# Kernel optimization log

Hardware: AMD Instinct MI355X
Metric: run time of the kernel (lower is better)

## Reference

```python
import jax, jax.numpy as jnp
import numpy as np

N = 4096
F = 256
E = 65536
NEG = -1e30  # mask value for non-neighbors in distance top-k


def setup_inputs() -> dict:
    key = jax.random.key(0)
    k1, k2, k3, k4, k5 = jax.random.split(key, 5)
    edge_index = jax.random.randint(k1, (2, E), 0, N)
    edge_weight = jax.random.uniform(k2, (E,), dtype=jnp.float32)
    features = jax.random.normal(k3, (N, F), dtype=jnp.float32)
    theta_1 = jax.random.uniform(k4, (1,), dtype=jnp.float32)
    theta_2 = jax.random.uniform(k5, (1,), dtype=jnp.float32)
    return {"edge_index": edge_index, "edge_weight": edge_weight,
            "features": features, "theta_1": theta_1, "theta_2": theta_2}


def reference(edge_index, edge_weight, features, theta_1, theta_2):
    n = features.shape[0]
    row, col = edge_index[0], edge_index[1]
    # Adjacency construction is done on detached numpy in the original.
    w = jax.lax.stop_gradient(edge_weight)
    X = jax.lax.stop_gradient(features)
    # sp.csr_matrix sums duplicate (i,j) entries -> scatter-add; + I; clamp >1 to 1
    A = jnp.zeros((n, n), jnp.float32).at[row, col].add(w)
    A = A + jnp.eye(n, dtype=jnp.float32)
    A = jnp.where(A > 1.0, 1.0, A)
    A2 = A @ A  # adjs[1] = sp_A ** 2
    # generate_sparse_ids mutates both A and A_robust(=A2 for r=2) with setdiag(0)
    off = 1.0 - jnp.eye(n, dtype=jnp.float32)
    A = A * off
    A2 = A2 * off
    D = jnp.sum(A != 0.0, axis=1)    # per-node degree (count_nonzero)
    Dr = jnp.sum(A2 != 0.0, axis=1)  # robust (2-hop) degree
    Df = D.astype(jnp.float32)
    d_thres = jnp.mean(Df) + 2.0 * jnp.std(Df)  # euclidean metric branch
    # squared-euclidean distances via gram trick: ||xu - xv||^2
    sq = jnp.sum(X * X, axis=1)
    dist2 = sq[:, None] + sq[None, :] - 2.0 * (X @ X.T)
    nbr2 = A2 != 0.0  # A_robust neighbors (diag excluded, already zeroed)
    dmask = jnp.where(nbr2, dist2, NEG)
    # rank of each candidate in descending-distance order (stable argsort)
    order = jnp.argsort(-dmask, axis=1)
    rank = jnp.argsort(order, axis=1)
    # nz_sel = D_r[u] - round(sparse_rate * D[u]) with sparse_rate=2.0 (exact ints)
    nz_sel = Dr - 2 * D
    # faithful to numpy argsort()[-0:] which selects ALL neighbors when nz_sel==0
    nz_eff = jnp.where(nz_sel == 0, n, nz_sel)
    Z_sparse = nbr2 & (rank < nz_eff[:, None])  # top nz_sel farthest neighbors
    Z_high = A == 0.0  # highD branch: zero all non-1-hop-neighbors
    highD = Df > d_thres
    nosparse = (~highD) & (2 * D > Dr)  # empty sparse_ids branch
    Z = jnp.where(highD[:, None], Z_high,
                  jnp.where(nosparse[:, None], False, Z_sparse))
    adj_k = jnp.where(Z, 0.0, A2 - A)  # diag already zero in both
    vals = theta_1 * edge_weight + theta_2 * jax.lax.stop_gradient(adj_k[row, col])
    return jnp.clip(vals, 0.0, None)
```

## Files before the change

### kernel.cpp

```cpp
#include <hip/hip_runtime.h>

#define NN 4096
#define FF 256
#define EE 65536
#define MAXDEG 64
#define MAXEPR 256
#define NCAND 2048

__device__ __forceinline__ int wred_sum(int v) {
#pragma unroll
    for (int o = 32; o >= 1; o >>= 1) v += __shfl_xor(v, o);
    return v;
}

__global__ void k_scatter(const int* __restrict__ ei, int* __restrict__ ecnt,
                          int* __restrict__ elist) {
    int e = blockIdx.x * blockDim.x + threadIdx.x;
    if (e >= EE) return;
    int r = ei[e];
    int p = atomicAdd(&ecnt[r], 1);
    if (p < MAXEPR) elist[r * MAXEPR + p] = e;
}

__global__ void k_build(const int* __restrict__ ei, const float* __restrict__ ew,
                        const int* __restrict__ ecnt, const int* __restrict__ elist,
                        const float* __restrict__ X,
                        unsigned short* __restrict__ ccol, float* __restrict__ cval,
                        int* __restrict__ deg, double* __restrict__ sq) {
    __shared__ float row[NN];
    __shared__ int cnt;
    const int u = blockIdx.x;
    const int tid = threadIdx.x;
    const int lane = tid & 63;
    const unsigned long long lmask = (1ull << lane) - 1ull;

    for (int i = tid; i < NN; i += 256) row[i] = 0.f;
    if (tid == 0) cnt = 0;
    __syncthreads();

    int ne = ecnt[u]; if (ne > MAXEPR) ne = MAXEPR;
    for (int i = tid; i < ne; i += 256) {
        int e = elist[u * MAXEPR + i];
        int c = ei[EE + e];
        if (c != u) atomicAdd(&row[c], ew[e]);
    }
    __syncthreads();

    for (int i = tid; i < NN; i += 256) {
        float w = row[i];
        bool nzf = (w != 0.f);
        unsigned long long m = __ballot(nzf);
        int base = 0;
        if (lane == 0 && m) base = atomicAdd(&cnt, __popcll(m));
        base = __shfl(base, 0);
        int pos = base + __popcll(m & lmask);
        if (nzf && pos < MAXDEG) {
            ccol[u * MAXDEG + pos] = (unsigned short)i;
            cval[u * MAXDEG + pos] = fminf(w, 1.f);
        }
    }
    __syncthreads();
    if (tid == 0) deg[u] = cnt;

    if (tid < 64) {
        float4 x4 = ((const float4*)(X + (size_t)u * FF))[lane];
        double s = (double)x4.x * x4.x + (double)x4.y * x4.y +
                   (double)x4.z * x4.z + (double)x4.w * x4.w;
#pragma unroll
        for (int o = 32; o >= 1; o >>= 1) s += __shfl_xor(s, o);
        if (lane == 0) sq[u] = s;
    }
}

__global__ void k_stats(const int* __restrict__ deg, double* __restrict__ thres) {
    __shared__ double sd[256], sd2[256];
    int t = threadIdx.x;
    double s = 0, s2 = 0;
    for (int i = t; i < NN; i += 256) {
        double d = (double)deg[i];
        s += d; s2 += d * d;
    }
    sd[t] = s; sd2[t] = s2;
    __syncthreads();
    for (int o = 128; o >= 1; o >>= 1) {
        if (t < o) { sd[t] += sd[t + o]; sd2[t] += sd2[t + o]; }
        __syncthreads();
    }
    if (t == 0) {
        double mean = sd[0] / NN;
        double var = sd2[0] / NN - mean * mean;
        if (var < 0) var = 0;
        thres[0] = mean + 2.0 * sqrt(var);
    }
}

__launch_bounds__(256, 5)
__global__ void k_main(const int* __restrict__ ei, const float* __restrict__ ew,
                       const float* __restrict__ X, const float* __restrict__ th1p,
                       const float* __restrict__ th2p,
                       const unsigned short* __restrict__ ccol,
                       const float* __restrict__ cval, const int* __restrict__ deg,
                       const int* __restrict__ ecnt, const int* __restrict__ elist,
                       const double* __restrict__ sq, const double* __restrict__ thresp,
                       float* __restrict__ out) {
    __shared__ float acc[NN];
    __shared__ float Xu[FF];
    __shared__ unsigned short cidx[NCAND];
    __shared__ float cdist[NCAND];
    __shared__ unsigned short Aucol[MAXDEG];
    __shared__ float Auval[MAXDEG];
    __shared__ int ncand;

    const int u = blockIdx.x;
    const int tid = threadIdx.x;
    const int lane = tid & 63;
    const int wave = tid >> 6;
    const unsigned long long lmask = (1ull << lane) - 1ull;

    const int du = deg[u];
    const int dul = min(du, MAXDEG);
    for (int i = tid; i < NN; i += 256) acc[i] = 0.f;
    if (tid < FF / 4)
        ((float4*)Xu)[tid] = ((const float4*)(X + (size_t)u * FF))[tid];
    if (tid >= 128 && tid - 128 < dul) {
        Aucol[tid - 128] = ccol[u * MAXDEG + tid - 128];
        Auval[tid - 128] = cval[u * MAXDEG + tid - 128];
    }
    if (tid == 0) ncand = 0;
    __syncthreads();

    for (int kk = wave; kk <= dul; kk += 4) {
        int k; float wuk;
        if (kk == dul) { k = u; wuk = 1.f; }
        else { k = Aucol[kk]; wuk = Auval[kk]; }
        int dkl = min(deg[k], MAXDEG);
        for (int j = lane; j <= dkl; j += 64) {
            int v; float wkv;
            if (j == dkl) { v = k; wkv = 1.f; }
            else { v = ccol[k * MAXDEG + j]; wkv = cval[k * MAXDEG + j]; }
            atomicAdd(&acc[v], wuk * wkv);
        }
    }
    __syncthreads();
    if (tid == 0) acc[u] = 0.f;
    __syncthreads();

    for (int i = tid; i < NN; i += 256) {
        bool nzf = (acc[i] != 0.f);
        unsigned long long m = __ballot(nzf);
        int base = 0;
        if (lane == 0 && m) base = atomicAdd(&ncand, __popcll(m));
        base = __shfl(base, 0);
        int pos = base + __popcll(m & lmask);
        if (nzf && pos < NCAND) cidx[pos] = (unsigned short)i;
    }
    __syncthreads();
    const int Dr = ncand;
    const int Drs = min(Dr, NCAND);

    const double squ = sq[u];
    for (int c = tid; c < Drs; c += 256) {
        int v = cidx[c];
        const float4* __restrict__ Xv = (const float4*)(X + (size_t)v * FF);
        double sqv = sq[v];
        double s0 = 0, s1 = 0, s2 = 0, s3 = 0;
#pragma unroll 2
        for (int f = 0; f < FF / 4; f += 4) {
            float4 a0 = Xv[f + 0], a1 = Xv[f + 1], a2 = Xv[f + 2], a3 = Xv[f + 3];
            float4 b0 = ((const float4*)Xu)[f + 0];
            float4 b1 = ((const float4*)Xu)[f + 1];
            float4 b2 = ((const float4*)Xu)[f + 2];
            float4 b3 = ((const float4*)Xu)[f + 3];
            s0 += (double)a0.x * b0.x + (double)a0.y * b0.y +
                  (double)a0.z * b0.z + (double)a0.w * b0.w;
            s1 += (double)a1.x * b1.x + (double)a1.y * b1.y +
                  (double)a1.z * b1.z + (double)a1.w * b1.w;
            s2 += (double)a2.x * b2.x + (double)a2.y * b2.y +
                  (double)a2.z * b2.z + (double)a2.w * b2.w;
            s3 += (double)a3.x * b3.x + (double)a3.y * b3.y +
                  (double)a3.z * b3.z + (double)a3.w * b3.w;
        }
        cdist[c] = (float)(squ + sqv - 2.0 * (s0 + s1 + s2 + s3));
    }
    __syncthreads();

    const int D = du;
    const bool highD = ((double)D > thresp[0]);
    const int nz = Dr - 2 * D;
    const float th1 = th1p[0], th2 = th2p[0];
    int ne = ecnt[u]; if (ne > MAXEPR) ne = MAXEPR;
    for (int idx = wave; idx < ne; idx += 4) {
        int e = elist[u * MAXEPR + idx];
        int v = ei[EE + e];
        float w = ew[e];
        float a2v = acc[v];
        float avl = 0.f;
        bool hit = false;
        for (int t = lane; t < dul; t += 64)
            if ((int)Aucol[t] == v) { avl = Auval[t]; hit = true; }
        unsigned long long hm = __ballot(hit);
        float av = hm ? __shfl(avl, (int)__builtin_ctzll(hm)) : 0.f;
        float adj;
        if (highD) {
            adj = (av != 0.f) ? (a2v - av) : 0.f;
        } else if (nz < 0) {
            adj = a2v - av;
        } else if (nz == 0) {
            adj = 0.f;
        } else if (a2v == 0.f) {
            adj = 0.f;
        } else {
            float dvl = 0.f; bool fnd = false;
            for (int c = lane; c < Drs; c += 64)
                if ((int)cidx[c] == v) { dvl = cdist[c]; fnd = true; }
            unsigned long long fm = __ballot(fnd);
            float dv = __shfl(dvl, (int)__builtin_ctzll(fm));
            int cnt = 0;
            for (int c = lane; c < Drs; c += 64) {
                float cd = cdist[c];
                int ci = cidx[c];
                cnt += (cd > dv || (cd == dv && ci < v)) ? 1 : 0;
            }
            cnt = wred_sum(cnt);
            adj = (cnt < nz) ? 0.f : (a2v - av);
        }
        if (lane == 0) out[e] = fmaxf(0.f, fmaf(th1, w, th2 * adj));
    }
}

extern "C" void kernel_launch(void* const* d_in, const int* in_sizes, int n_in,
                              void* d_out, int out_size, void* d_ws, size_t ws_size,
                              hipStream_t stream) {
    const int* ei = (const int*)d_in[0];
    const float* ew = (const float*)d_in[1];
    const float* X = (const float*)d_in[2];
    const float* th1 = (const float*)d_in[3];
    const float* th2 = (const float*)d_in[4];
    float* out = (float*)d_out;

    char* ws = (char*)d_ws;
    size_t off = 0;
    unsigned short* ccol = (unsigned short*)(ws + off); off += (size_t)NN * MAXDEG * 2;
    float* cval = (float*)(ws + off);         off += (size_t)NN * MAXDEG * 4;
    int* deg = (int*)(ws + off);              off += (size_t)NN * 4;
    int* ecnt = (int*)(ws + off);             off += (size_t)NN * 4;
    double* sq = (double*)(ws + off);         off += (size_t)NN * 8;
    double* thres = (double*)(ws + off);      off += 256;
    int* elist = (int*)(ws + off);            off += (size_t)NN * MAXEPR * 4;

    hipMemsetAsync(ecnt, 0, (size_t)NN * 4, stream);

    k_scatter<<<EE / 256, 256, 0, stream>>>(ei, ecnt, elist);
    k_build<<<NN, 256, 0, stream>>>(ei, ew, ecnt, elist, X, ccol, cval, deg, sq);
    k_stats<<<1, 256, 0, stream>>>(deg, thres);
    k_main<<<NN, 256, 0, stream>>>(ei, ew, X, th1, th2, ccol, cval, deg,
                                   ecnt, elist, sq, thres, out);
}
```

Before: 277.5 us.

## Split main kernel into A² pass and distance-rank pass, sparsify row build

The single main kernel is split into k_a2, which computes 2-hop counts, candidate lists and the edge outputs for the common branches, and k_dist, which runs only for nodes that need the distance top-k ranking and exits early otherwise. k_build now uses 64 threads per block and touches only the adjacency slots it uses, instead of clearing and scanning a dense 4096-entry shared row. The goal is less shared memory and higher occupancy in the A² pass, and skipping the costly FP64 distance work for most nodes. In exchange, candidate lists and partial results go through global workspace, and NCAND is halved to 1024, which could truncate candidates for nodes with large 2-hop degree.

New measurement: 272.3 us, median of 2. No clear change (-1.9%).

```diff
diff --git a/kernel.cpp b/kernel.cpp
--- a/kernel.cpp
+++ b/kernel.cpp
@@ -5,9 +5,14 @@
 #define EE 65536
 #define MAXDEG 64
 #define MAXEPR 256
-#define NCAND 2048
+#define NCAND 1024
 
 __device__ __forceinline__ int wred_sum(int v) {
+#pragma unroll
+    for (int o = 32; o >= 1; o >>= 1) v += __shfl_xor(v, o);
+    return v;
+}
+__device__ __forceinline__ double wred_dsum(double v) {
 #pragma unroll
     for (int o = 32; o >= 1; o >>= 1) v += __shfl_xor(v, o);
     return v;
@@ -30,46 +35,42 @@
     __shared__ float row[NN];
     __shared__ int cnt;
     const int u = blockIdx.x;
-    const int tid = threadIdx.x;
-    const int lane = tid & 63;
-    const unsigned long long lmask = (1ull << lane) - 1ull;
-
-    for (int i = tid; i < NN; i += 256) row[i] = 0.f;
-    if (tid == 0) cnt = 0;
-    __syncthreads();
+    const int lane = threadIdx.x;
+    if (lane == 0) cnt = 0;
 
     int ne = ecnt[u]; if (ne > MAXEPR) ne = MAXEPR;
-    for (int i = tid; i < ne; i += 256) {
+    for (int i = lane; i < ne; i += 64) {
+        int c = ei[EE + elist[u * MAXEPR + i]];
+        if (c != u) row[c] = 0.f;
+    }
+    __syncthreads();
+    for (int i = lane; i < ne; i += 64) {
         int e = elist[u * MAXEPR + i];
         int c = ei[EE + e];
         if (c != u) atomicAdd(&row[c], ew[e]);
     }
     __syncthreads();
-
-    for (int i = tid; i < NN; i += 256) {
-        float w = row[i];
-        bool nzf = (w != 0.f);
-        unsigned long long m = __ballot(nzf);
-        int base = 0;
-        if (lane == 0 && m) base = atomicAdd(&cnt, __popcll(m));
-        base = __shfl(base, 0);
-        int pos = base + __popcll(m & lmask);
-        if (nzf && pos < MAXDEG) {
-            ccol[u * MAXDEG + pos] = (unsigned short)i;
-            cval[u * MAXDEG + pos] = fminf(w, 1.f);
-        }
-    }
-    __syncthreads();
-    if (tid == 0) deg[u] = cnt;
-
-    if (tid < 64) {
-        float4 x4 = ((const float4*)(X + (size_t)u * FF))[lane];
-        double s = (double)x4.x * x4.x + (double)x4.y * x4.y +
-                   (double)x4.z * x4.z + (double)x4.w * x4.w;
-#pragma unroll
-        for (int o = 32; o >= 1; o >>= 1) s += __shfl_xor(s, o);
-        if (lane == 0) sq[u] = s;
-    }
+    for (int i = lane; i < ne; i += 64) {
+        int c = ei[EE + elist[u * MAXEPR + i]];
+        if (c != u) {
+            float w = atomicExch(&row[c], 0.f);
+            if (w != 0.f) {
+                int p = atomicAdd(&cnt, 1);
+                if (p < MAXDEG) {
+                    ccol[u * MAXDEG + p] = (unsigned short)c;
+                    cval[u * MAXDEG + p] = fminf(w, 1.f);
+                }
+            }
+        }
+    }
+    __syncthreads();
+    if (lane == 0) deg[u] = cnt;
+
+    float4 x4 = ((const float4*)(X + (size_t)u * FF))[lane];
+    double s = (double)x4.x * x4.x + (double)x4.y * x4.y +
+               (double)x4.z * x4.z + (double)x4.w * x4.w;
+    s = wred_dsum(s);
+    if (lane == 0) sq[u] = s;
 }
 
 __global__ void k_stats(const int* __restrict__ deg, double* __restrict__ thres) {
@@ -94,19 +95,17 @@
     }
 }
 
-__launch_bounds__(256, 5)
-__global__ void k_main(const int* __restrict__ ei, const float* __restrict__ ew,
-                       const float* __restrict__ X, const float* __restrict__ th1p,
-                       const float* __restrict__ th2p,
-                       const unsigned short* __restrict__ ccol,
-                       const float* __restrict__ cval, const int* __restrict__ deg,
-                       const int* __restrict__ ecnt, const int* __restrict__ elist,
-                       const double* __restrict__ sq, const double* __restrict__ thresp,
-                       float* __restrict__ out) {
+__launch_bounds__(256, 8)
+__global__ void k_a2(const int* __restrict__ ei, const float* __restrict__ ew,
+                     const float* __restrict__ th1p, const float* __restrict__ th2p,
+                     const unsigned short* __restrict__ ccol,
+                     const float* __restrict__ cval, const int* __restrict__ deg,
+                     const int* __restrict__ ecnt, const int* __restrict__ elist,
+                     const double* __restrict__ thresp,
+                     unsigned short* __restrict__ cidx_g, int* __restrict__ drg,
+                     int* __restrict__ nzg, float* __restrict__ eadj,
+                     float* __restrict__ out) {
     __shared__ float acc[NN];
-    __shared__ float Xu[FF];
-    __shared__ unsigned short cidx[NCAND];
-    __shared__ float cdist[NCAND];
     __shared__ unsigned short Aucol[MAXDEG];
     __shared__ float Auval[MAXDEG];
     __shared__ int ncand;
@@ -119,12 +118,11 @@
 
     const int du = deg[u];
     const int dul = min(du, MAXDEG);
-    for (int i = tid; i < NN; i += 256) acc[i] = 0.f;
-    if (tid < FF / 4)
-        ((float4*)Xu)[tid] = ((const float4*)(X + (size_t)u * FF))[tid];
-    if (tid >= 128 && tid - 128 < dul) {
-        Aucol[tid - 128] = ccol[u * MAXDEG + tid - 128];
-        Auval[tid - 128] = cval[u * MAXDEG + tid - 128];
+    for (int i = tid; i < NN / 4; i += 256)
+        ((float4*)acc)[i] = make_float4(0.f, 0.f, 0.f, 0.f);
+    if (tid < dul) {
+        Aucol[tid] = ccol[u * MAXDEG + tid];
+        Auval[tid] = cval[u * MAXDEG + tid];
     }
     if (tid == 0) ncand = 0;
     __syncthreads();
@@ -145,85 +143,121 @@
     if (tid == 0) acc[u] = 0.f;
     __syncthreads();
 
-    for (int i = tid; i < NN; i += 256) {
-        bool nzf = (acc[i] != 0.f);
-        unsigned long long m = __ballot(nzf);
-        int base = 0;
-        if (lane == 0 && m) base = atomicAdd(&ncand, __popcll(m));
-        base = __shfl(base, 0);
-        int pos = base + __popcll(m & lmask);
-        if (nzf && pos < NCAND) cidx[pos] = (unsigned short)i;
+    for (int i4 = tid; i4 < NN / 4; i4 += 256) {
+        float4 a4 = ((float4*)acc)[i4];
+        float e4[4] = {a4.x, a4.y, a4.z, a4.w};
+#pragma unroll
+        for (int j = 0; j < 4; ++j) {
+            bool nzf = (e4[j] != 0.f);
+            unsigned long long m = __ballot(nzf);
+            int base = 0;
+            if (lane == 0 && m) base = atomicAdd(&ncand, __popcll(m));
+            base = __shfl(base, 0);
+            int pos = base + __popcll(m & lmask);
+            if (nzf && pos < NCAND) cidx_g[u * NCAND + pos] = (unsigned short)(i4 * 4 + j);
+        }
     }
     __syncthreads();
     const int Dr = ncand;
-    const int Drs = min(Dr, NCAND);
+
+    const bool highD = ((double)du > thresp[0]);
+    const int nz = Dr - 2 * du;
+    const bool rankcase = (!highD) && (nz > 0);
+    const float th1 = th1p[0], th2 = th2p[0];
+    if (tid == 0) {
+        drg[u] = min(Dr, NCAND);
+        nzg[u] = rankcase ? nz : 0;
+    }
+
+    int ne = ecnt[u]; if (ne > MAXEPR) ne = MAXEPR;
+    for (int idx = wave; idx < ne; idx += 4) {
+        int e = elist[u * MAXEPR + idx];
+        int v = ei[EE + e];
+        float w = ew[e];
+        float a2v = acc[v];
+        float avl = 0.f; bool hit = false;
+        for (int t = lane; t < dul; t += 64)
+            if ((int)Aucol[t] == v) { avl = Auval[t]; hit = true; }
+        unsigned long long hm = __ballot(hit);
+        float av = hm ? __shfl(avl, (int)__builtin_ctzll(hm)) : 0.f;
+        if (rankcase) {
+            if (lane == 0) eadj[u * MAXEPR + idx] = a2v - av;
+        } else {
+            float adj;
+            if (highD)       adj = (av != 0.f) ? (a2v - av) : 0.f;
+            else if (nz < 0) adj = a2v - av;
+            else             adj = 0.f;
+            if (lane == 0) out[e] = fmaxf(0.f, fmaf(th1, w, th2 * adj));
+        }
+    }
+}
+
+__launch_bounds__(256, 8)
+__global__ void k_dist(const int* __restrict__ ei, const float* __restrict__ ew,
+                       const float* __restrict__ X, const float* __restrict__ th1p,
+                       const float* __restrict__ th2p,
+                       const int* __restrict__ ecnt, const int* __restrict__ elist,
+                       const double* __restrict__ sq,
+                       const unsigned short* __restrict__ cidx_g,
+                       const int* __restrict__ drg, const int* __restrict__ nzg,
+                       const float* __restrict__ eadj, float* __restrict__ out) {
+    __shared__ float Xu[FF];
+    __shared__ unsigned short cidx[NCAND];
+    __shared__ float cdist[NCAND];
+
+    const int u = blockIdx.x;
+    const int nz = nzg[u];
+    if (nz <= 0) return;
+    const int tid = threadIdx.x;
+    const int lane = tid & 63;
+    const int wave = tid >> 6;
+
+    const int Drs = drg[u];
+    if (tid < FF / 4)
+        ((float4*)Xu)[tid] = ((const float4*)(X + (size_t)u * FF))[tid];
+    for (int i = tid; i < Drs; i += 256) cidx[i] = cidx_g[u * NCAND + i];
+    __syncthreads();
 
     const double squ = sq[u];
     for (int c = tid; c < Drs; c += 256) {
         int v = cidx[c];
         const float4* __restrict__ Xv = (const float4*)(X + (size_t)v * FF);
         double sqv = sq[v];
-        double s0 = 0, s1 = 0, s2 = 0, s3 = 0;
-#pragma unroll 2
-        for (int f = 0; f < FF / 4; f += 4) {
-            float4 a0 = Xv[f + 0], a1 = Xv[f + 1], a2 = Xv[f + 2], a3 = Xv[f + 3];
-            float4 b0 = ((const float4*)Xu)[f + 0];
-            float4 b1 = ((const float4*)Xu)[f + 1];
-            float4 b2 = ((const float4*)Xu)[f + 2];
-            float4 b3 = ((const float4*)Xu)[f + 3];
-            s0 += (double)a0.x * b0.x + (double)a0.y * b0.y +
-                  (double)a0.z * b0.z + (double)a0.w * b0.w;
-            s1 += (double)a1.x * b1.x + (double)a1.y * b1.y +
-                  (double)a1.z * b1.z + (double)a1.w * b1.w;
-            s2 += (double)a2.x * b2.x + (double)a2.y * b2.y +
-                  (double)a2.z * b2.z + (double)a2.w * b2.w;
-            s3 += (double)a3.x * b3.x + (double)a3.y * b3.y +
-                  (double)a3.z * b3.z + (double)a3.w * b3.w;
-        }
-        cdist[c] = (float)(squ + sqv - 2.0 * (s0 + s1 + s2 + s3));
-    }
-    __syncthreads();
-
-    const int D = du;
-    const bool highD = ((double)D > thresp[0]);
-    const int nz = Dr - 2 * D;
+        double s0 = 0.0, s1 = 0.0;
+#pragma unroll 4
+        for (int f = 0; f < FF / 4; f += 2) {
+            float4 a = Xv[f];
+            float4 b = ((const float4*)Xu)[f];
+            s0 += (double)a.x * b.x + (double)a.y * b.y +
+                  (double)a.z * b.z + (double)a.w * b.w;
+            float4 p = Xv[f + 1];
+            float4 q = ((const float4*)Xu)[f + 1];
+            s1 += (double)p.x * q.x + (double)p.y * q.y +
+                  (double)p.z * q.z + (double)p.w * q.w;
+        }
+        cdist[c] = (float)(squ + sqv - 2.0 * (s0 + s1));
+    }
+    __syncthreads();
+
     const float th1 = th1p[0], th2 = th2p[0];
     int ne = ecnt[u]; if (ne > MAXEPR) ne = MAXEPR;
     for (int idx = wave; idx < ne; idx += 4) {
         int e = elist[u * MAXEPR + idx];
         int v = ei[EE + e];
         float w = ew[e];
-        float a2v = acc[v];
-        float avl = 0.f;
-        bool hit = false;
-        for (int t = lane; t < dul; t += 64)
-            if ((int)Aucol[t] == v) { avl = Auval[t]; hit = true; }
-        unsigned long long hm = __ballot(hit);
-        float av = hm ? __shfl(avl, (int)__builtin_ctzll(hm)) : 0.f;
-        float adj;
-        if (highD) {
-            adj = (av != 0.f) ? (a2v - av) : 0.f;
-        } else if (nz < 0) {
-            adj = a2v - av;
-        } else if (nz == 0) {
-            adj = 0.f;
-        } else if (a2v == 0.f) {
-            adj = 0.f;
-        } else {
-            float dvl = 0.f; bool fnd = false;
-            for (int c = lane; c < Drs; c += 64)
-                if ((int)cidx[c] == v) { dvl = cdist[c]; fnd = true; }
-            unsigned long long fm = __ballot(fnd);
-            float dv = __shfl(dvl, (int)__builtin_ctzll(fm));
-            int cnt = 0;
-            for (int c = lane; c < Drs; c += 64) {
-                float cd = cdist[c];
-                int ci = cidx[c];
-                cnt += (cd > dv || (cd == dv && ci < v)) ? 1 : 0;
-            }
-            cnt = wred_sum(cnt);
-            adj = (cnt < nz) ? 0.f : (a2v - av);
-        }
+        float dvl = 0.f; bool fnd = false;
+        for (int c = lane; c < Drs; c += 64)
+            if ((int)cidx[c] == v) { dvl = cdist[c]; fnd = true; }
+        unsigned long long fm = __ballot(fnd);
+        float dv = __shfl(dvl, (int)__builtin_ctzll(fm));
+        int cnt = 0;
+        for (int c = lane; c < Drs; c += 64) {
+            float cd = cdist[c];
+            int ci = cidx[c];
+            cnt += (cd > dv || (cd == dv && ci < v)) ? 1 : 0;
+        }
+        cnt = wred_sum(cnt);
+        float adj = (cnt < nz) ? 0.f : eadj[u * MAXEPR + idx];
         if (lane == 0) out[e] = fmaxf(0.f, fmaf(th1, w, th2 * adj));
     }
 }
@@ -241,18 +275,24 @@
     char* ws = (char*)d_ws;
     size_t off = 0;
     unsigned short* ccol = (unsigned short*)(ws + off); off += (size_t)NN * MAXDEG * 2;
-    float* cval = (float*)(ws + off);         off += (size_t)NN * MAXDEG * 4;
-    int* deg = (int*)(ws + off);              off += (size_t)NN * 4;
-    int* ecnt = (int*)(ws + off);             off += (size_t)NN * 4;
-    double* sq = (double*)(ws + off);         off += (size_t)NN * 8;
-    double* thres = (double*)(ws + off);      off += 256;
-    int* elist = (int*)(ws + off);            off += (size_t)NN * MAXEPR * 4;
+    float* cval = (float*)(ws + off);          off += (size_t)NN * MAXDEG * 4;
+    int* deg = (int*)(ws + off);               off += (size_t)NN * 4;
+    int* ecnt = (int*)(ws + off);              off += (size_t)NN * 4;
+    double* sq = (double*)(ws + off);          off += (size_t)NN * 8;
+    double* thres = (double*)(ws + off);       off += 256;
+    int* elist = (int*)(ws + off);             off += (size_t)NN * MAXEPR * 4;
+    unsigned short* cidx_g = (unsigned short*)(ws + off); off += (size_t)NN * NCAND * 2;
+    int* drg = (int*)(ws + off);               off += (size_t)NN * 4;
+    int* nzg = (int*)(ws + off);               off += (size_t)NN * 4;
+    float* eadj = (float*)(ws + off);          off += (size_t)NN * MAXEPR * 4;
 
     hipMemsetAsync(ecnt, 0, (size_t)NN * 4, stream);
 
     k_scatter<<<EE / 256, 256, 0, stream>>>(ei, ecnt, elist);
-    k_build<<<NN, 256, 0, stream>>>(ei, ew, ecnt, elist, X, ccol, cval, deg, sq);
+    k_build<<<NN, 64, 0, stream>>>(ei, ew, ecnt, elist, X, ccol, cval, deg, sq);
     k_stats<<<1, 256, 0, stream>>>(deg, thres);
-    k_main<<<NN, 256, 0, stream>>>(ei, ew, X, th1, th2, ccol, cval, deg,
-                                   ecnt, elist, sq, thres, out);
-}
+    k_a2<<<NN, 256, 0, stream>>>(ei, ew, th1, th2, ccol, cval, deg, ecnt, elist,
+                                 thres, cidx_g, drg, nzg, eadj, out);
+    k_dist<<<NN, 256, 0, stream>>>(ei, ew, X, th1, th2, ecnt, elist, sq,
+                                   cidx_g, drg, nzg, eadj, out);
+}
```
